# Optimization experiments

Hardware: AMD Instinct MI355X
Metric: run time of the kernel (lower is better)

The kernel has to match this reference:

```python
import jax, jax.numpy as jnp
import numpy as np

N = 200      # num_of_node
P = 200      # num_of_pattern
TOPK = 3
STRIDE = 25
B = 32
T = 9000     # S * STRIDE with S = 360
H = 128      # classifier hidden


def setup_inputs() -> dict:
    key = jax.random.key(0)
    k0, k1, k2, k3 = jax.random.split(key, 4)
    x = jax.random.normal(k0, (B, N, T), dtype=jnp.float32)
    # xavier_uniform-ish scale, gain 1.414
    patterns = jax.random.normal(k1, (P, N), dtype=jnp.float32) * np.float32(1.414 * np.sqrt(2.0 / (P + N)))
    W1 = jax.random.normal(k2, (N, H), dtype=jnp.float32) * np.float32(np.sqrt(2.0 / N))
    b1 = jnp.zeros((H,), jnp.float32)
    W2 = jax.random.normal(k3, (H, 2), dtype=jnp.float32) * np.float32(np.sqrt(2.0 / H))
    b2 = jnp.zeros((2,), jnp.float32)
    return {"x": x, "length": 9000, "patterns": patterns,
            "W1": W1, "b1": b1, "W2": W2, "b2": b2}


def _forward(x, patterns, W1, b1, W2, b2, length):
    Bx = x.shape[0]
    S = length // STRIDE                     # size_after_pool (static int)
    eye = jnp.eye(N, dtype=x.dtype)
    # patterns = tanh(patterns * (1 - I)) + I, then L2-normalize rows
    p = jnp.tanh(patterns * (1.0 - eye)) + eye
    np_ = p / jnp.sqrt((p ** 2).sum(-1, keepdims=True) + 1e-9)          # [P,N]
    # MRI_length_regularize: crop and transpose -> [B,T,N]
    frames = jnp.swapaxes(x[:, :, :S * STRIDE], 1, 2)
    nf = frames / jnp.sqrt((frames ** 2).sum(-1, keepdims=True) + 1e-9)  # [B,T,N]
    # cosine similarity frame vs pattern
    scores = jnp.einsum('btn,pn->btp', nf, np_)                          # [B,T,P]
    # MaxPool1d(stride, stride, return_indices=True) on [B,P,T]
    sw = jnp.swapaxes(scores, 1, 2).reshape(Bx, P, S, STRIDE)
    posscores = sw.max(-1)                                               # [B,P,S]
    negscores = (-sw).max(-1)
    offs = jnp.arange(S) * STRIDE
    pos_idx = jax.lax.stop_gradient(jnp.argmax(sw, -1) + offs)           # [B,P,S] global indices
    neg_idx = jax.lax.stop_gradient(jnp.argmax(-sw, -1) + offs)
    # scatter +1/-1 into signal_select [B,P,T]; indices unique per (b,p) row
    bidx = jnp.arange(Bx)[:, None, None]
    pidx = jnp.arange(P)[None, :, None]
    ss = jnp.zeros((Bx, P, S * STRIDE), x.dtype)
    ss = ss.at[bidx, pidx, pos_idx].add(1.0)
    ss = ss.at[bidx, pidx, neg_idx].add(-1.0)
    Sf = jnp.asarray(S, x.dtype)
    avg_sel = np.float32(np.sqrt(200.0 / TOPK)) * jnp.einsum('bpt,btn->bpn', ss, nf) / Sf / 2.0
    compos = (posscores / Sf).sum(-1)                                    # [B,P]
    comneg = (negscores / Sf).sum(-1)
    finalscore = (compos + comneg) / 2.0
    # top_select on normalized patterns (abs topK mask per row)
    idx = jax.lax.top_k(jnp.abs(np_), TOPK)[1]                           # [P,K]
    mask = jnp.zeros((P, N), x.dtype).at[jnp.arange(P)[:, None], idx].set(1.0)
    tp = mask * np_                                                      # toppattern [P,N]
    Tframe = avg_sel * mask                                              # [B,P,N]
    scores2 = ((Tframe / jnp.sqrt((Tframe ** 2).sum(-1, keepdims=True) + 1e-9)) *
               (tp / jnp.sqrt((tp ** 2).sum(-1, keepdims=True) + 1e-9))).sum(-1)  # [B,P]
    # SigLoss: Frobenius norms
    norm = (1.0 - jnp.sqrt((tp ** 2).sum()) / jnp.sqrt((np_ ** 2).sum())) ** 2
    # realpattern: sign(toppattern)/topK, detached
    rp = jax.lax.stop_gradient(jnp.sign(tp) / TOPK)                      # [P,N]
    non_diag = jnp.ones((N, N), x.dtype) * TOPK - eye * (TOPK - 1)
    diag = finalscore + 0.25 * (scores2 * np.float32(np.sqrt(TOPK / 200.0)))
    graphs = jnp.einsum('pn,bp,pm->bnm', rp, diag, rp) * non_diag / (TOPK / 5.0)  # [B,N,N]
    # Graph_Analysis('ae') stand-in classifier: per-node MLP + mean pool + linear head
    h = jax.nn.relu(graphs @ W1 + b1)                                    # [B,N,H]
    out = h.mean(1) @ W2 + b2                                            # [B,2]
    return out, norm, graphs


def reference(x, length, patterns, W1, b1, W2, b2):
    return _forward(x, patterns, W1, b1, W2, b2, length)
```

## Files before the change

kernel.cpp:

```cpp
#include <hip/hip_runtime.h>
#include <math.h>

namespace {

constexpr int kN = 200;
constexpr int kP = 200;
constexpr int kT = 9000;
constexpr int kB = 32;
constexpr int kS = 360;
constexpr int kH = 128;
constexpr int kWC = 72;


__device__ inline float wave_sum(float v) {
#pragma unroll
  for (int off = 32; off >= 1; off >>= 1) v += __shfl_xor(v, off);
  return v;
}

__global__ __launch_bounds__(64) void k_pattern(
    const float* __restrict__ pat, float* __restrict__ npm,
    float* __restrict__ t3val, int* __restrict__ t3idx,
    float* __restrict__ t3sign, float* __restrict__ ssq_tp,
    float* __restrict__ gsums) {
  const int p = blockIdx.x, lane = threadIdx.x;
  __shared__ float row[kN];
  float v[4];
  float ssq = 0.f;
#pragma unroll
  for (int j = 0; j < 4; ++j) {
    int n = lane + 64 * j;
    float val = 0.f;
    if (n < kN) {
      float a = pat[p * kN + n];
      val = (n == p) ? 1.0f : tanhf(a);
    }
    v[j] = val;
    ssq += val * val;
  }
  ssq = wave_sum(ssq);
  const float inv = 1.0f / sqrtf(ssq + 1e-9f);
  float ssqn = 0.f;
#pragma unroll
  for (int j = 0; j < 4; ++j) {
    int n = lane + 64 * j;
    if (n < kN) {
      float nv = v[j] * inv;
      npm[p * kN + n] = nv;
      row[n] = nv;
      ssqn += nv * nv;
    }
  }
  ssqn = wave_sum(ssqn);
  __syncthreads();
  if (lane == 0) {
    float v1 = -1.f, v2 = -1.f, v3 = -1.f;
    int i1 = 0, i2 = 0, i3 = 0;
    for (int n = 0; n < kN; ++n) {
      float a = fabsf(row[n]);
      if (a > v1)      { v3 = v2; i3 = i2; v2 = v1; i2 = i1; v1 = a; i1 = n; }
      else if (a > v2) { v3 = v2; i3 = i2; v2 = a; i2 = n; }
      else if (a > v3) { v3 = a; i3 = n; }
    }
    float a1 = row[i1], a2 = row[i2], a3 = row[i3];
    t3idx[p * 3 + 0] = i1; t3idx[p * 3 + 1] = i2; t3idx[p * 3 + 2] = i3;
    t3val[p * 3 + 0] = a1; t3val[p * 3 + 1] = a2; t3val[p * 3 + 2] = a3;
    t3sign[p * 3 + 0] = (a1 > 0.f) ? 1.f : ((a1 < 0.f) ? -1.f : 0.f);
    t3sign[p * 3 + 1] = (a2 > 0.f) ? 1.f : ((a2 < 0.f) ? -1.f : 0.f);
    t3sign[p * 3 + 2] = (a3 > 0.f) ? 1.f : ((a3 < 0.f) ? -1.f : 0.f);
    float st = a1 * a1 + a2 * a2 + a3 * a3;
    ssq_tp[p] = st;
    atomicAdd(&gsums[0], ssqn);
    atomicAdd(&gsums[1], st);
  }
}

__global__ __launch_bounds__(256) void k_rownorm(const float* __restrict__ x,
                                                 float* __restrict__ inv_rn) {
  int idx = blockIdx.x * 256 + threadIdx.x;
  if (idx >= kB * kT) return;
  int b = idx / kT, t = idx % kT;
  const float* xp = x + (size_t)b * kN * kT + t;
  float s0 = 0.f, s1 = 0.f, s2 = 0.f, s3 = 0.f;
  for (int n = 0; n < kN; n += 4) {
    float x0 = xp[(size_t)(n + 0) * kT];
    float x1 = xp[(size_t)(n + 1) * kT];
    float x2 = xp[(size_t)(n + 2) * kT];
    float x3 = xp[(size_t)(n + 3) * kT];
    s0 += x0 * x0; s1 += x1 * x1; s2 += x2 * x2; s3 += x3 * x3;
  }
  float s = (s0 + s1) + (s2 + s3);
  inv_rn[idx] = 1.0f / sqrtf(s + 1e-9f);
}

__global__ __launch_bounds__(512, 2) void k_scores_pool(
    const float* __restrict__ x, const float* __restrict__ npm,
    const float* __restrict__ inv_rn,
    float* __restrict__ posval, float* __restrict__ negval,
    unsigned short* __restrict__ posi, unsigned short* __restrict__ negi) {
  const int bid = blockIdx.x;
  const int b = bid / kWC, wc = bid % kWC;
  const int t0 = wc * 125;
  __shared__ float ps[kP * 51];
  __shared__ float xs[50 * 140];
  const int tid = threadIdx.x;
  const int p2 = tid % 100, w = tid / 100;
  const bool active = tid < 500;
  float accA[25], accB[25];
#pragma unroll
  for (int t = 0; t < 25; ++t) { accA[t] = 0.f; accB[t] = 0.f; }
  const size_t xb = (size_t)b * kN * kT;

  for (int nc = 0; nc < 4; ++nc) {
    __syncthreads();
    for (int i = tid; i < kP * 50; i += 512) {
      int p = i / 50, n = i % 50;
      ps[p * 51 + n] = npm[p * kN + nc * 50 + n];
    }
    for (int i = tid; i < 50 * 125; i += 512) {
      int n = i / 125, tt = i % 125;
      xs[n * 140 + (tt / 25) * 28 + (tt % 25)] =
          x[xb + (size_t)(nc * 50 + n) * kT + t0 + tt];
    }
    __syncthreads();
    if (active) {
      for (int n = 0; n < 50; ++n) {
        float va = ps[p2 * 51 + n];
        float vb = ps[(p2 + 100) * 51 + n];
        const float* xr = &xs[n * 140 + w * 28];
#pragma unroll
        for (int t = 0; t < 25; ++t) {
          float xv = xr[t];
          accA[t] = fmaf(va, xv, accA[t]);
          accB[t] = fmaf(vb, xv, accB[t]);
        }
      }
    }
  }

  if (active) {
    const int tg0 = t0 + w * 25;
    float bA = -1e30f, bnA = -1e30f, bB = -1e30f, bnB = -1e30f;
    int iA = 0, inA = 0, iB = 0, inB = 0;
#pragma unroll
    for (int t = 0; t < 25; ++t) {
      float iv = inv_rn[b * kT + tg0 + t];
      float sA = accA[t] * iv, sB = accB[t] * iv;
      if (sA > bA)   { bA = sA;  iA = t; }
      if (-sA > bnA) { bnA = -sA; inA = t; }
      if (sB > bB)   { bB = sB;  iB = t; }
      if (-sB > bnB) { bnB = -sB; inB = t; }
    }
    const int s = wc * 5 + w;
    const size_t oA = (size_t)(b * kP + p2) * kS + s;
    const size_t oB = (size_t)(b * kP + p2 + 100) * kS + s;
    posval[oA] = bA;  negval[oA] = bnA;
    posval[oB] = bB;  negval[oB] = bnB;
    posi[oA] = (unsigned short)(tg0 + iA);
    negi[oA] = (unsigned short)(tg0 + inA);
    posi[oB] = (unsigned short)(tg0 + iB);
    negi[oB] = (unsigned short)(tg0 + inB);
  }
}

__global__ __launch_bounds__(256) void k_avgsel(
    const float* __restrict__ x, const float* __restrict__ inv_rn,
    const unsigned short* __restrict__ posi, const unsigned short* __restrict__ negi,
    const float* __restrict__ posval, const float* __restrict__ negval,
    const int* __restrict__ t3idx, const float* __restrict__ t3val,
    const float* __restrict__ ssq_tp, float* __restrict__ diag) {
  const int gw = blockIdx.x * 4 + (threadIdx.x >> 6);
  const int lane = threadIdx.x & 63;
  const int b = gw / kP, p = gw % kP;
  const int n0 = t3idx[p * 3 + 0], n1 = t3idx[p * 3 + 1], n2 = t3idx[p * 3 + 2];
  const float* xb = x + (size_t)b * kN * kT;
  const float* ivb = inv_rn + b * kT;
  const size_t base = (size_t)(b * kP + p) * kS;
  float a0 = 0.f, a1 = 0.f, a2 = 0.f, sp = 0.f, sn = 0.f;
  for (int s = lane; s < kS; s += 64) {
    int tp_ = posi[base + s], tn_ = negi[base + s];
    float ivp = ivb[tp_], ivn = ivb[tn_];
    a0 += xb[(size_t)n0 * kT + tp_] * ivp - xb[(size_t)n0 * kT + tn_] * ivn;
    a1 += xb[(size_t)n1 * kT + tp_] * ivp - xb[(size_t)n1 * kT + tn_] * ivn;
    a2 += xb[(size_t)n2 * kT + tp_] * ivp - xb[(size_t)n2 * kT + tn_] * ivn;
    sp += posval[base + s];
    sn += negval[base + s];
  }
  a0 = wave_sum(a0); a1 = wave_sum(a1); a2 = wave_sum(a2);
  sp = wave_sum(sp); sn = wave_sum(sn);
  if (lane == 0) {
    const float c0 = 8.16496580927726f;
    float T0 = c0 * a0 / 360.0f / 2.0f;
    float T1 = c0 * a1 / 360.0f / 2.0f;
    float T2 = c0 * a2 / 360.0f / 2.0f;
    float st = T0 * T0 + T1 * T1 + T2 * T2;
    float itf = 1.0f / sqrtf(st + 1e-9f);
    float itp = 1.0f / sqrtf(ssq_tp[p] + 1e-9f);
    float s2 = T0 * itf * (t3val[p * 3 + 0] * itp) +
               T1 * itf * (t3val[p * 3 + 1] * itp) +
               T2 * itf * (t3val[p * 3 + 2] * itp);
    float fs = (sp / 360.0f + sn / 360.0f) * 0.5f;
    diag[b * kP + p] = fs + 0.25f * (s2 * 0.12247448713915890f);
  }
}

__global__ __launch_bounds__(256) void k_graphs(
    const float* __restrict__ diag, const int* __restrict__ t3idx,
    const float* __restrict__ t3sign, float* __restrict__ gout) {
  const int b = blockIdx.x, tid = threadIdx.x;
  __shared__ float g[kN * kN];
  for (int i = tid; i < kN * kN; i += 256) g[i] = 0.f;
  __syncthreads();
  for (int p = tid; p < kP; p += 256) {
    float d = diag[b * kP + p];
    int i0 = t3idx[p * 3 + 0], i1 = t3idx[p * 3 + 1], i2 = t3idx[p * 3 + 2];
    float r0 = t3sign[p * 3 + 0] * (1.0f / 3.0f);
    float r1 = t3sign[p * 3 + 1] * (1.0f / 3.0f);
    float r2 = t3sign[p * 3 + 2] * (1.0f / 3.0f);
    int   ii[3] = {i0, i1, i2};
    float rr[3] = {r0, r1, r2};
#pragma unroll
    for (int j = 0; j < 3; ++j)
#pragma unroll
      for (int k = 0; k < 3; ++k)
        atomicAdd(&g[ii[j] * kN + ii[k]], d * rr[j] * rr[k]);
  }
  __syncthreads();
  float* go = gout + (size_t)b * kN * kN;
  for (int i = tid; i < kN * kN; i += 256) {
    int n = i / kN, m = i % kN;
    float nd = (n == m) ? 1.0f : 3.0f;
    go[i] = g[i] * nd / 0.6f;
  }
}

__global__ __launch_bounds__(256) void k_classifier(
    const float* __restrict__ graphs, const float* __restrict__ W1,
    const float* __restrict__ b1, float* __restrict__ meanh) {
  const int b = blockIdx.x / 8, nc = blockIdx.x % 8;
  const int tid = threadIdx.x;
  __shared__ float g[25][kN];
  for (int i = tid; i < 25 * kN; i += 256) {
    int n = i / kN, m = i % kN;
    g[n][m] = graphs[(size_t)b * kN * kN + (size_t)(nc * 25 + n) * kN + m];
  }
  __syncthreads();
  const int hh = tid & 127, grp = tid >> 7;
  const int ns = (grp == 0) ? 0 : 13, ne = (grp == 0) ? 13 : 25;
  float sumh = 0.f;
  for (int n = ns; n < ne; ++n) {
    float acc = b1[hh];
    for (int m = 0; m < kN; ++m) acc = fmaf(g[n][m], W1[m * kH + hh], acc);
    sumh += fmaxf(acc, 0.f);
  }
  atomicAdd(&meanh[b * kH + hh], sumh);
}

__global__ __launch_bounds__(64) void k_final(
    const float* __restrict__ meanh, const float* __restrict__ W2,
    const float* __restrict__ b2, const float* __restrict__ gsums,
    float* __restrict__ out) {
  const int tid = threadIdx.x;
  if (tid < 64) {
    int b = tid >> 1, k = tid & 1;
    float acc = 0.f;
    for (int h = 0; h < kH; ++h) {
      float mv = meanh[b * kH + h] / 200.0f;
      acc = fmaf(mv, W2[h * 2 + k], acc);
    }
    out[b * 2 + k] = acc + b2[k];
  }
  if (tid == 0) {
    float r = 1.0f - sqrtf(gsums[1]) / sqrtf(gsums[0]);
    out[64] = r * r;
  }
}

}

extern "C" void kernel_launch(void* const* d_in, const int* in_sizes, int n_in,
                              void* d_out, int out_size, void* d_ws, size_t ws_size,
                              hipStream_t stream) {
  const float* x   = (const float*)d_in[0];
  const float* pat = (const float*)d_in[2];
  const float* W1  = (const float*)d_in[3];
  const float* b1  = (const float*)d_in[4];
  const float* W2  = (const float*)d_in[5];
  const float* b2  = (const float*)d_in[6];
  float* out = (float*)d_out;

  char* ws = (char*)d_ws;
  float* meanh  = (float*)(ws + 0);
  float* gsums  = (float*)(ws + 16384);
  float* diag   = (float*)(ws + 16400);
  float* ssqtp  = (float*)(ws + 42000);
  float* t3val  = (float*)(ws + 42800);
  float* t3sign = (float*)(ws + 45200);
  int*   t3idx  = (int*)(ws + 47600);
  float* npm    = (float*)(ws + 50000);
  float* invrn  = (float*)(ws + 210000);
  float* posval = (float*)(ws + 1362000);
  float* negval = (float*)(ws + 10578000);
  unsigned short* posi = (unsigned short*)(ws + 19794000);
  unsigned short* negi = (unsigned short*)(ws + 24402000);

  hipMemsetAsync(d_ws, 0, 16392, stream);
  k_pattern<<<kP, 64, 0, stream>>>(pat, npm, t3val, t3idx, t3sign, ssqtp, gsums);
  k_rownorm<<<(kB * kT) / 256, 256, 0, stream>>>(x, invrn);
  k_scores_pool<<<kB * kWC, 512, 0, stream>>>(x, npm, invrn, posval, negval, posi, negi);
  k_avgsel<<<(kB * kP) / 4, 256, 0, stream>>>(x, invrn, posi, negi, posval, negval,
                                              t3idx, t3val, ssqtp, diag);
  k_graphs<<<kB, 256, 0, stream>>>(diag, t3idx, t3sign, out + 65);
  k_classifier<<<kB * 8, 256, 0, stream>>>(out + 65, W1, b1, meanh);
  k_final<<<1, 64, 0, stream>>>(meanh, W2, b2, gsums, out);
}
```

Measured before the change: 902.5 us.

## Retile score+pool GEMM to 125-register tiles and fuse pooled sums via atomics

Rewrites the score and max-pool kernel so each thread accumulates a 25-pattern by 5-time register tile. Operands are loaded from transposed, float4-friendly shared layouts, and the pattern matrix is now stored transposed. Pooled max and min values are reduced with shuffles and summed into per-(b,p) accumulators with atomics, which drops the large posval/negval buffers and the re-read of them in avgsel. The graph kernel becomes a direct global atomic scatter after a memset of the output, replacing the per-batch shared-memory build and full write. The 125-float accumulator raises register pressure and may lower occupancy. Float atomics also make the sum order nondeterministic.

```diff
diff --git a/kernel.cpp b/kernel.cpp
--- a/kernel.cpp
+++ b/kernel.cpp
@@ -9,7 +9,6 @@
 constexpr int kB = 32;
 constexpr int kS = 360;
 constexpr int kH = 128;
-constexpr int kWC = 72;
 
 
 __device__ inline float wave_sum(float v) {
@@ -19,7 +18,7 @@
 }
 
 __global__ __launch_bounds__(64) void k_pattern(
-    const float* __restrict__ pat, float* __restrict__ npm,
+    const float* __restrict__ pat, float* __restrict__ npmT,
     float* __restrict__ t3val, int* __restrict__ t3idx,
     float* __restrict__ t3sign, float* __restrict__ ssq_tp,
     float* __restrict__ gsums) {
@@ -46,7 +45,7 @@
     int n = lane + 64 * j;
     if (n < kN) {
       float nv = v[j] * inv;
-      npm[p * kN + n] = nv;
+      npmT[n * kP + p] = nv;
       row[n] = nv;
       ssqn += nv * nv;
     }
@@ -93,80 +92,130 @@
   inv_rn[idx] = 1.0f / sqrtf(s + 1e-9f);
 }
 
-__global__ __launch_bounds__(512, 2) void k_scores_pool(
-    const float* __restrict__ x, const float* __restrict__ npm,
+__global__ __launch_bounds__(256) void k_scores_pool2(
+    const float* __restrict__ x, const float* __restrict__ npmT,
     const float* __restrict__ inv_rn,
-    float* __restrict__ posval, float* __restrict__ negval,
-    unsigned short* __restrict__ posi, unsigned short* __restrict__ negi) {
+    unsigned short* __restrict__ posi, unsigned short* __restrict__ negi,
+    float* __restrict__ compos, float* __restrict__ comneg) {
   const int bid = blockIdx.x;
-  const int b = bid / kWC, wc = bid % kWC;
-  const int t0 = wc * 125;
-  __shared__ float ps[kP * 51];
-  __shared__ float xs[50 * 140];
+  const int pg = bid & 1;
+  const int tc = (bid >> 1) % 30;
+  const int b  = bid / 60;
+  const int t0 = tc * 300;
   const int tid = threadIdx.x;
-  const int p2 = tid % 100, w = tid / 100;
-  const bool active = tid < 500;
-  float accA[25], accB[25];
-#pragma unroll
-  for (int t = 0; t < 25; ++t) { accA[t] = 0.f; accB[t] = 0.f; }
-  const size_t xb = (size_t)b * kN * kT;
-
-  for (int nc = 0; nc < 4; ++nc) {
+  const int wid = tid >> 6, lane = tid & 63;
+
+  __shared__ float xs[20 * 64 * 8];
+  __shared__ float ps[20 * 4 * 28];
+  __shared__ float ivs[300];
+
+  for (int i = tid; i < 300; i += 256) ivs[i] = inv_rn[b * kT + t0 + i];
+
+  float acc[125];
+#pragma unroll
+  for (int i = 0; i < 125; ++i) acc[i] = 0.f;
+
+  const size_t xb = (size_t)b * kN * kT + t0;
+
+  for (int c = 0; c < 10; ++c) {
     __syncthreads();
-    for (int i = tid; i < kP * 50; i += 512) {
-      int p = i / 50, n = i % 50;
-      ps[p * 51 + n] = npm[p * kN + nc * 50 + n];
-    }
-    for (int i = tid; i < 50 * 125; i += 512) {
-      int n = i / 125, tt = i % 125;
-      xs[n * 140 + (tt / 25) * 28 + (tt % 25)] =
-          x[xb + (size_t)(nc * 50 + n) * kT + t0 + tt];
+    for (int i = tid; i < 20 * 300; i += 256) {
+      int n = i / 300, tt = i % 300;
+      xs[n * 512 + (tt / 5) * 8 + (tt % 5)] =
+          x[xb + (size_t)(c * 20 + n) * kT + tt];
+    }
+    for (int i = tid; i < 20 * 100; i += 256) {
+      int n = i / 100, pp = i % 100;
+      ps[n * 112 + (pp / 25) * 28 + (pp % 25)] =
+          npmT[(c * 20 + n) * kP + pg * 100 + pp];
     }
     __syncthreads();
-    if (active) {
-      for (int n = 0; n < 50; ++n) {
-        float va = ps[p2 * 51 + n];
-        float vb = ps[(p2 + 100) * 51 + n];
-        const float* xr = &xs[n * 140 + w * 28];
-#pragma unroll
-        for (int t = 0; t < 25; ++t) {
-          float xv = xr[t];
-          accA[t] = fmaf(va, xv, accA[t]);
-          accB[t] = fmaf(vb, xv, accB[t]);
+    for (int n = 0; n < 20; ++n) {
+      const float4 x4 = *(const float4*)&xs[n * 512 + lane * 8];
+      const float xv4 = xs[n * 512 + lane * 8 + 4];
+      const float* pr = &ps[n * 112 + wid * 28];
+#pragma unroll
+      for (int g = 0; g < 6; ++g) {
+        const float4 p4 = *(const float4*)&pr[g * 4];
+        {
+          const float pv = p4.x; const int o = (g * 4 + 0) * 5;
+          acc[o+0]=fmaf(pv,x4.x,acc[o+0]); acc[o+1]=fmaf(pv,x4.y,acc[o+1]);
+          acc[o+2]=fmaf(pv,x4.z,acc[o+2]); acc[o+3]=fmaf(pv,x4.w,acc[o+3]);
+          acc[o+4]=fmaf(pv,xv4,acc[o+4]);
         }
-      }
-    }
-  }
-
-  if (active) {
-    const int tg0 = t0 + w * 25;
-    float bA = -1e30f, bnA = -1e30f, bB = -1e30f, bnB = -1e30f;
-    int iA = 0, inA = 0, iB = 0, inB = 0;
-#pragma unroll
-    for (int t = 0; t < 25; ++t) {
-      float iv = inv_rn[b * kT + tg0 + t];
-      float sA = accA[t] * iv, sB = accB[t] * iv;
-      if (sA > bA)   { bA = sA;  iA = t; }
-      if (-sA > bnA) { bnA = -sA; inA = t; }
-      if (sB > bB)   { bB = sB;  iB = t; }
-      if (-sB > bnB) { bnB = -sB; inB = t; }
-    }
-    const int s = wc * 5 + w;
-    const size_t oA = (size_t)(b * kP + p2) * kS + s;
-    const size_t oB = (size_t)(b * kP + p2 + 100) * kS + s;
-    posval[oA] = bA;  negval[oA] = bnA;
-    posval[oB] = bB;  negval[oB] = bnB;
-    posi[oA] = (unsigned short)(tg0 + iA);
-    negi[oA] = (unsigned short)(tg0 + inA);
-    posi[oB] = (unsigned short)(tg0 + iB);
-    negi[oB] = (unsigned short)(tg0 + inB);
+        {
+          const float pv = p4.y; const int o = (g * 4 + 1) * 5;
+          acc[o+0]=fmaf(pv,x4.x,acc[o+0]); acc[o+1]=fmaf(pv,x4.y,acc[o+1]);
+          acc[o+2]=fmaf(pv,x4.z,acc[o+2]); acc[o+3]=fmaf(pv,x4.w,acc[o+3]);
+          acc[o+4]=fmaf(pv,xv4,acc[o+4]);
+        }
+        {
+          const float pv = p4.z; const int o = (g * 4 + 2) * 5;
+          acc[o+0]=fmaf(pv,x4.x,acc[o+0]); acc[o+1]=fmaf(pv,x4.y,acc[o+1]);
+          acc[o+2]=fmaf(pv,x4.z,acc[o+2]); acc[o+3]=fmaf(pv,x4.w,acc[o+3]);
+          acc[o+4]=fmaf(pv,xv4,acc[o+4]);
+        }
+        {
+          const float pv = p4.w; const int o = (g * 4 + 3) * 5;
+          acc[o+0]=fmaf(pv,x4.x,acc[o+0]); acc[o+1]=fmaf(pv,x4.y,acc[o+1]);
+          acc[o+2]=fmaf(pv,x4.z,acc[o+2]); acc[o+3]=fmaf(pv,x4.w,acc[o+3]);
+          acc[o+4]=fmaf(pv,xv4,acc[o+4]);
+        }
+      }
+      {
+        const float pv = pr[24]; const int o = 24 * 5;
+        acc[o+0]=fmaf(pv,x4.x,acc[o+0]); acc[o+1]=fmaf(pv,x4.y,acc[o+1]);
+        acc[o+2]=fmaf(pv,x4.z,acc[o+2]); acc[o+3]=fmaf(pv,x4.w,acc[o+3]);
+        acc[o+4]=fmaf(pv,xv4,acc[o+4]);
+      }
+    }
+  }
+
+  if (lane < 60) {
+    const int w = lane / 5;
+    const int k5 = lane % 5;
+    float iv[5];
+#pragma unroll
+    for (int j = 0; j < 5; ++j) iv[j] = ivs[lane * 5 + j];
+    const int sidx = tc * 12 + w;
+    const int pwbase = pg * 100 + wid * 25;
+#pragma unroll
+    for (int pp = 0; pp < 25; ++pp) {
+      float mv = -1e30f, nv = 1e30f;
+      int mi = 0, ni = 0;
+#pragma unroll
+      for (int j = 0; j < 5; ++j) {
+        float s = acc[pp * 5 + j] * iv[j];
+        if (s > mv) { mv = s; mi = lane * 5 + j; }
+        if (s < nv) { nv = s; ni = lane * 5 + j; }
+      }
+      float bmv = -1e30f, bnv = 1e30f;
+      int bmi = 0, bni = 0;
+#pragma unroll
+      for (int k = 0; k < 5; ++k) {
+        float v  = __shfl(mv, w * 5 + k);
+        int   vi = __shfl(mi, w * 5 + k);
+        float u  = __shfl(nv, w * 5 + k);
+        int   ui = __shfl(ni, w * 5 + k);
+        if (v > bmv) { bmv = v; bmi = vi; }
+        if (u < bnv) { bnv = u; bni = ui; }
+      }
+      if (k5 == 0) {
+        const int p = pwbase + pp;
+        const size_t o = (size_t)(b * kP + p) * kS + sidx;
+        posi[o] = (unsigned short)(t0 + bmi);
+        negi[o] = (unsigned short)(t0 + bni);
+        atomicAdd(&compos[b * kP + p], bmv);
+        atomicAdd(&comneg[b * kP + p], -bnv);
+      }
+    }
   }
 }
 
 __global__ __launch_bounds__(256) void k_avgsel(
     const float* __restrict__ x, const float* __restrict__ inv_rn,
     const unsigned short* __restrict__ posi, const unsigned short* __restrict__ negi,
-    const float* __restrict__ posval, const float* __restrict__ negval,
+    const float* __restrict__ compos, const float* __restrict__ comneg,
     const int* __restrict__ t3idx, const float* __restrict__ t3val,
     const float* __restrict__ ssq_tp, float* __restrict__ diag) {
   const int gw = blockIdx.x * 4 + (threadIdx.x >> 6);
@@ -176,18 +225,15 @@
   const float* xb = x + (size_t)b * kN * kT;
   const float* ivb = inv_rn + b * kT;
   const size_t base = (size_t)(b * kP + p) * kS;
-  float a0 = 0.f, a1 = 0.f, a2 = 0.f, sp = 0.f, sn = 0.f;
+  float a0 = 0.f, a1 = 0.f, a2 = 0.f;
   for (int s = lane; s < kS; s += 64) {
     int tp_ = posi[base + s], tn_ = negi[base + s];
     float ivp = ivb[tp_], ivn = ivb[tn_];
     a0 += xb[(size_t)n0 * kT + tp_] * ivp - xb[(size_t)n0 * kT + tn_] * ivn;
     a1 += xb[(size_t)n1 * kT + tp_] * ivp - xb[(size_t)n1 * kT + tn_] * ivn;
     a2 += xb[(size_t)n2 * kT + tp_] * ivp - xb[(size_t)n2 * kT + tn_] * ivn;
-    sp += posval[base + s];
-    sn += negval[base + s];
   }
   a0 = wave_sum(a0); a1 = wave_sum(a1); a2 = wave_sum(a2);
-  sp = wave_sum(sp); sn = wave_sum(sn);
   if (lane == 0) {
     const float c0 = 8.16496580927726f;
     float T0 = c0 * a0 / 360.0f / 2.0f;
@@ -199,39 +245,33 @@
     float s2 = T0 * itf * (t3val[p * 3 + 0] * itp) +
                T1 * itf * (t3val[p * 3 + 1] * itp) +
                T2 * itf * (t3val[p * 3 + 2] * itp);
-    float fs = (sp / 360.0f + sn / 360.0f) * 0.5f;
+    float fs = (compos[b * kP + p] / 360.0f + comneg[b * kP + p] / 360.0f) * 0.5f;
     diag[b * kP + p] = fs + 0.25f * (s2 * 0.12247448713915890f);
   }
 }
 
-__global__ __launch_bounds__(256) void k_graphs(
+__global__ __launch_bounds__(256) void k_graphs_scatter(
     const float* __restrict__ diag, const int* __restrict__ t3idx,
     const float* __restrict__ t3sign, float* __restrict__ gout) {
-  const int b = blockIdx.x, tid = threadIdx.x;
-  __shared__ float g[kN * kN];
-  for (int i = tid; i < kN * kN; i += 256) g[i] = 0.f;
-  __syncthreads();
-  for (int p = tid; p < kP; p += 256) {
-    float d = diag[b * kP + p];
-    int i0 = t3idx[p * 3 + 0], i1 = t3idx[p * 3 + 1], i2 = t3idx[p * 3 + 2];
-    float r0 = t3sign[p * 3 + 0] * (1.0f / 3.0f);
-    float r1 = t3sign[p * 3 + 1] * (1.0f / 3.0f);
-    float r2 = t3sign[p * 3 + 2] * (1.0f / 3.0f);
-    int   ii[3] = {i0, i1, i2};
-    float rr[3] = {r0, r1, r2};
-#pragma unroll
-    for (int j = 0; j < 3; ++j)
-#pragma unroll
-      for (int k = 0; k < 3; ++k)
-        atomicAdd(&g[ii[j] * kN + ii[k]], d * rr[j] * rr[k]);
-  }
-  __syncthreads();
+  const int i = blockIdx.x * 256 + threadIdx.x;
+  if (i >= kB * kP) return;
+  const int b = i / kP, p = i % kP;
+  const float d = diag[i];
+  int   ii[3];
+  float rr[3];
+#pragma unroll
+  for (int j = 0; j < 3; ++j) {
+    ii[j] = t3idx[p * 3 + j];
+    rr[j] = t3sign[p * 3 + j] * (1.0f / 3.0f);
+  }
   float* go = gout + (size_t)b * kN * kN;
-  for (int i = tid; i < kN * kN; i += 256) {
-    int n = i / kN, m = i % kN;
-    float nd = (n == m) ? 1.0f : 3.0f;
-    go[i] = g[i] * nd / 0.6f;
-  }
+#pragma unroll
+  for (int j = 0; j < 3; ++j)
+#pragma unroll
+    for (int k = 0; k < 3; ++k) {
+      float nd = (ii[j] == ii[k]) ? 1.0f : 3.0f;
+      atomicAdd(&go[ii[j] * kN + ii[k]], d * rr[j] * rr[k] * nd * (1.0f / 0.6f));
+    }
 }
 
 __global__ __launch_bounds__(256) void k_classifier(
@@ -292,25 +332,29 @@
   char* ws = (char*)d_ws;
   float* meanh  = (float*)(ws + 0);
   float* gsums  = (float*)(ws + 16384);
-  float* diag   = (float*)(ws + 16400);
-  float* ssqtp  = (float*)(ws + 42000);
-  float* t3val  = (float*)(ws + 42800);
-  float* t3sign = (float*)(ws + 45200);
-  int*   t3idx  = (int*)(ws + 47600);
-  float* npm    = (float*)(ws + 50000);
-  float* invrn  = (float*)(ws + 210000);
-  float* posval = (float*)(ws + 1362000);
-  float* negval = (float*)(ws + 10578000);
-  unsigned short* posi = (unsigned short*)(ws + 19794000);
-  unsigned short* negi = (unsigned short*)(ws + 24402000);
-
-  hipMemsetAsync(d_ws, 0, 16392, stream);
-  k_pattern<<<kP, 64, 0, stream>>>(pat, npm, t3val, t3idx, t3sign, ssqtp, gsums);
-  k_rownorm<<<(kB * kT) / 256, 256, 0, stream>>>(x, invrn);
-  k_scores_pool<<<kB * kWC, 512, 0, stream>>>(x, npm, invrn, posval, negval, posi, negi);
-  k_avgsel<<<(kB * kP) / 4, 256, 0, stream>>>(x, invrn, posi, negi, posval, negval,
+  float* compos = (float*)(ws + 16400);
+  float* comneg = (float*)(ws + 42000);
+  float* diag   = (float*)(ws + 67600);
+  float* ssqtp  = (float*)(ws + 93200);
+  float* t3val  = (float*)(ws + 94000);
+  float* t3sign = (float*)(ws + 96400);
+  int*   t3idx  = (int*)(ws + 98800);
+  float* npmT   = (float*)(ws + 101200);
+  float* invrn  = (float*)(ws + 261200);
+  unsigned short* posi = (unsigned short*)(ws + 1413200);
+  unsigned short* negi = (unsigned short*)(ws + 6021200);
+
+  hipMemsetAsync(d_ws, 0, 67600, stream);
+  hipMemsetAsync((char*)d_out + 65 * 4, 0, (size_t)kB * kN * kN * 4, stream);
+
+  k_pattern<<<kP, 64, 0, stream>>>(pat, npmT, t3val, t3idx, t3sign, ssqtp, gsums);
+  k_rownorm<<<(kB * kT + 255) / 256, 256, 0, stream>>>(x, invrn);
+  k_scores_pool2<<<kB * 30 * 2, 256, 0, stream>>>(x, npmT, invrn, posi, negi,
+                                                  compos, comneg);
+  k_avgsel<<<(kB * kP) / 4, 256, 0, stream>>>(x, invrn, posi, negi, compos, comneg,
                                               t3idx, t3val, ssqtp, diag);
-  k_graphs<<<kB, 256, 0, stream>>>(diag, t3idx, t3sign, out + 65);
+  k_graphs_scatter<<<(kB * kP + 255) / 256, 256, 0, stream>>>(diag, t3idx, t3sign,
+                                                              out + 65);
   k_classifier<<<kB * 8, 256, 0, stream>>>(out + 65, W1, b1, meanh);
   k_final<<<1, 64, 0, stream>>>(meanh, W2, b2, gsums, out);
 }
```

Result: slower. 1.676 ms (+85.6%).

## Fuse row-norm, score pooling and selection averaging into one scores kernel

Applied to the files above, without the earlier changes.

Removes the separate row-norm pass over x by accumulating squared sums in shared memory while x tiles are staged. The pooled argmax/argmin results are consumed in place: each block gathers the top-3 node values and accumulates pooled sums into shared buffers, then flushes them with global atomics. This drops the large posval/negval/posi/negi intermediates and the avgsel kernel. The graph build becomes a per-(b,p) global atomic scatter onto a memset output. The costs are added shared-memory atomics during tile loading, the loss of the two-blocks-per-CU launch bound, and float-atomic ordering nondeterminism.

```diff
diff --git a/kernel.cpp b/kernel.cpp
--- a/kernel.cpp
+++ b/kernel.cpp
@@ -9,7 +9,6 @@
 constexpr int kB = 32;
 constexpr int kS = 360;
 constexpr int kH = 128;
-constexpr int kWC = 72;
 
 
 __device__ inline float wave_sum(float v) {
@@ -75,41 +74,34 @@
   }
 }
 
-__global__ __launch_bounds__(256) void k_rownorm(const float* __restrict__ x,
-                                                 float* __restrict__ inv_rn) {
-  int idx = blockIdx.x * 256 + threadIdx.x;
-  if (idx >= kB * kT) return;
-  int b = idx / kT, t = idx % kT;
-  const float* xp = x + (size_t)b * kN * kT + t;
-  float s0 = 0.f, s1 = 0.f, s2 = 0.f, s3 = 0.f;
-  for (int n = 0; n < kN; n += 4) {
-    float x0 = xp[(size_t)(n + 0) * kT];
-    float x1 = xp[(size_t)(n + 1) * kT];
-    float x2 = xp[(size_t)(n + 2) * kT];
-    float x3 = xp[(size_t)(n + 3) * kT];
-    s0 += x0 * x0; s1 += x1 * x1; s2 += x2 * x2; s3 += x3 * x3;
-  }
-  float s = (s0 + s1) + (s2 + s3);
-  inv_rn[idx] = 1.0f / sqrtf(s + 1e-9f);
-}
-
-__global__ __launch_bounds__(512, 2) void k_scores_pool(
+__global__ __launch_bounds__(512) void k_scores_fused(
     const float* __restrict__ x, const float* __restrict__ npm,
-    const float* __restrict__ inv_rn,
-    float* __restrict__ posval, float* __restrict__ negval,
-    unsigned short* __restrict__ posi, unsigned short* __restrict__ negi) {
+    const int* __restrict__ t3idx,
+    float* __restrict__ asumG, float* __restrict__ cposG,
+    float* __restrict__ cnegG) {
   const int bid = blockIdx.x;
-  const int b = bid / kWC, wc = bid % kWC;
+  const int b = bid / 72, wc = bid % 72;
   const int t0 = wc * 125;
   __shared__ float ps[kP * 51];
   __shared__ float xs[50 * 140];
+  __shared__ float ssq[128];
+  __shared__ float asumL[kP * 3];
+  __shared__ float cposL[kP];
+  __shared__ float cnegL[kP];
+  __shared__ int   t3iL[kP * 3];
   const int tid = threadIdx.x;
   const int p2 = tid % 100, w = tid / 100;
   const bool active = tid < 500;
+
+  for (int i = tid; i < kP * 3; i += 512) { asumL[i] = 0.f; t3iL[i] = t3idx[i]; }
+  for (int i = tid; i < kP; i += 512) { cposL[i] = 0.f; cnegL[i] = 0.f; }
+  for (int i = tid; i < 128; i += 512) ssq[i] = 0.f;
+
   float accA[25], accB[25];
 #pragma unroll
   for (int t = 0; t < 25; ++t) { accA[t] = 0.f; accB[t] = 0.f; }
-  const size_t xb = (size_t)b * kN * kT;
+  const size_t xbase = (size_t)b * kN * kT;
+  const size_t xb = xbase + t0;
 
   for (int nc = 0; nc < 4; ++nc) {
     __syncthreads();
@@ -119,8 +111,9 @@
     }
     for (int i = tid; i < 50 * 125; i += 512) {
       int n = i / 125, tt = i % 125;
-      xs[n * 140 + (tt / 25) * 28 + (tt % 25)] =
-          x[xb + (size_t)(nc * 50 + n) * kT + t0 + tt];
+      float v = x[xb + (size_t)(nc * 50 + n) * kT + tt];
+      xs[n * 140 + (tt / 25) * 28 + (tt % 25)] = v;
+      atomicAdd(&ssq[tt], v * v);
     }
     __syncthreads();
     if (active) {
@@ -140,98 +133,90 @@
 
   if (active) {
     const int tg0 = t0 + w * 25;
-    float bA = -1e30f, bnA = -1e30f, bB = -1e30f, bnB = -1e30f;
-    int iA = 0, inA = 0, iB = 0, inB = 0;
-#pragma unroll
-    for (int t = 0; t < 25; ++t) {
-      float iv = inv_rn[b * kT + tg0 + t];
-      float sA = accA[t] * iv, sB = accB[t] * iv;
-      if (sA > bA)   { bA = sA;  iA = t; }
-      if (-sA > bnA) { bnA = -sA; inA = t; }
-      if (sB > bB)   { bB = sB;  iB = t; }
-      if (-sB > bnB) { bnB = -sB; inB = t; }
-    }
-    const int s = wc * 5 + w;
-    const size_t oA = (size_t)(b * kP + p2) * kS + s;
-    const size_t oB = (size_t)(b * kP + p2 + 100) * kS + s;
-    posval[oA] = bA;  negval[oA] = bnA;
-    posval[oB] = bB;  negval[oB] = bnB;
-    posi[oA] = (unsigned short)(tg0 + iA);
-    negi[oA] = (unsigned short)(tg0 + inA);
-    posi[oB] = (unsigned short)(tg0 + iB);
-    negi[oB] = (unsigned short)(tg0 + inB);
-  }
-}
-
-__global__ __launch_bounds__(256) void k_avgsel(
-    const float* __restrict__ x, const float* __restrict__ inv_rn,
-    const unsigned short* __restrict__ posi, const unsigned short* __restrict__ negi,
-    const float* __restrict__ posval, const float* __restrict__ negval,
-    const int* __restrict__ t3idx, const float* __restrict__ t3val,
+    float iv[25];
+#pragma unroll
+    for (int t = 0; t < 25; ++t) iv[t] = 1.0f / sqrtf(ssq[w * 25 + t] + 1e-9f);
+
+#define DO_HALF(ACC, PIDX)                                                    \
+    {                                                                         \
+      const int P_ = (PIDX);                                                  \
+      float bmv = -1e30f, bnv = 1e30f, ivp = 0.f, ivn = 0.f;                  \
+      int bmi = 0, bni = 0;                                                   \
+      _Pragma("unroll")                                                       \
+      for (int t = 0; t < 25; ++t) {                                          \
+        float s = ACC[t] * iv[t];                                             \
+        if (s > bmv) { bmv = s; bmi = t; ivp = iv[t]; }                       \
+        if (s < bnv) { bnv = s; bni = t; ivn = iv[t]; }                       \
+      }                                                                       \
+      atomicAdd(&cposL[P_], bmv);                                             \
+      atomicAdd(&cnegL[P_], -bnv);                     \
+      const int gp = tg0 + bmi, gn = tg0 + bni;                               \
+      _Pragma("unroll")                                                       \
+      for (int j = 0; j < 3; ++j) {                                           \
+        int nj = t3iL[P_ * 3 + j];                                            \
+        float xpv = x[xbase + (size_t)nj * kT + gp];                          \
+        float xnv = x[xbase + (size_t)nj * kT + gn];                          \
+        atomicAdd(&asumL[P_ * 3 + j], xpv * ivp - xnv * ivn);                 \
+      }                                                                       \
+    }
+
+    DO_HALF(accA, p2)
+    DO_HALF(accB, p2 + 100)
+#undef DO_HALF
+  }
+
+  __syncthreads();
+  for (int i = tid; i < kP * 5; i += 512) {
+    if (i < kP * 3)           atomicAdd(&asumG[b * kP * 3 + i], asumL[i]);
+    else if (i < kP * 4)      atomicAdd(&cposG[b * kP + (i - kP * 3)], cposL[i - kP * 3]);
+    else                      atomicAdd(&cnegG[b * kP + (i - kP * 4)], cnegL[i - kP * 4]);
+  }
+}
+
+__global__ __launch_bounds__(256) void k_diag(
+    const float* __restrict__ asumG, const float* __restrict__ cposG,
+    const float* __restrict__ cnegG, const float* __restrict__ t3val,
     const float* __restrict__ ssq_tp, float* __restrict__ diag) {
-  const int gw = blockIdx.x * 4 + (threadIdx.x >> 6);
-  const int lane = threadIdx.x & 63;
-  const int b = gw / kP, p = gw % kP;
-  const int n0 = t3idx[p * 3 + 0], n1 = t3idx[p * 3 + 1], n2 = t3idx[p * 3 + 2];
-  const float* xb = x + (size_t)b * kN * kT;
-  const float* ivb = inv_rn + b * kT;
-  const size_t base = (size_t)(b * kP + p) * kS;
-  float a0 = 0.f, a1 = 0.f, a2 = 0.f, sp = 0.f, sn = 0.f;
-  for (int s = lane; s < kS; s += 64) {
-    int tp_ = posi[base + s], tn_ = negi[base + s];
-    float ivp = ivb[tp_], ivn = ivb[tn_];
-    a0 += xb[(size_t)n0 * kT + tp_] * ivp - xb[(size_t)n0 * kT + tn_] * ivn;
-    a1 += xb[(size_t)n1 * kT + tp_] * ivp - xb[(size_t)n1 * kT + tn_] * ivn;
-    a2 += xb[(size_t)n2 * kT + tp_] * ivp - xb[(size_t)n2 * kT + tn_] * ivn;
-    sp += posval[base + s];
-    sn += negval[base + s];
-  }
-  a0 = wave_sum(a0); a1 = wave_sum(a1); a2 = wave_sum(a2);
-  sp = wave_sum(sp); sn = wave_sum(sn);
-  if (lane == 0) {
-    const float c0 = 8.16496580927726f;
-    float T0 = c0 * a0 / 360.0f / 2.0f;
-    float T1 = c0 * a1 / 360.0f / 2.0f;
-    float T2 = c0 * a2 / 360.0f / 2.0f;
-    float st = T0 * T0 + T1 * T1 + T2 * T2;
-    float itf = 1.0f / sqrtf(st + 1e-9f);
-    float itp = 1.0f / sqrtf(ssq_tp[p] + 1e-9f);
-    float s2 = T0 * itf * (t3val[p * 3 + 0] * itp) +
-               T1 * itf * (t3val[p * 3 + 1] * itp) +
-               T2 * itf * (t3val[p * 3 + 2] * itp);
-    float fs = (sp / 360.0f + sn / 360.0f) * 0.5f;
-    diag[b * kP + p] = fs + 0.25f * (s2 * 0.12247448713915890f);
-  }
-}
-
-__global__ __launch_bounds__(256) void k_graphs(
+  const int i = blockIdx.x * 256 + threadIdx.x;
+  if (i >= kB * kP) return;
+  const int p = i % kP;
+  const float c0 = 8.16496580927726f;
+  float a0 = asumG[i * 3 + 0], a1 = asumG[i * 3 + 1], a2 = asumG[i * 3 + 2];
+  float T0 = c0 * a0 / 360.0f / 2.0f;
+  float T1 = c0 * a1 / 360.0f / 2.0f;
+  float T2 = c0 * a2 / 360.0f / 2.0f;
+  float st = T0 * T0 + T1 * T1 + T2 * T2;
+  float itf = 1.0f / sqrtf(st + 1e-9f);
+  float itp = 1.0f / sqrtf(ssq_tp[p] + 1e-9f);
+  float s2 = T0 * itf * (t3val[p * 3 + 0] * itp) +
+             T1 * itf * (t3val[p * 3 + 1] * itp) +
+             T2 * itf * (t3val[p * 3 + 2] * itp);
+  float fs = (cposG[i] / 360.0f + cnegG[i] / 360.0f) * 0.5f;
+  diag[i] = fs + 0.25f * (s2 * 0.12247448713915890f);
+}
+
+__global__ __launch_bounds__(256) void k_graphs_scatter(
     const float* __restrict__ diag, const int* __restrict__ t3idx,
     const float* __restrict__ t3sign, float* __restrict__ gout) {
-  const int b = blockIdx.x, tid = threadIdx.x;
-  __shared__ float g[kN * kN];
-  for (int i = tid; i < kN * kN; i += 256) g[i] = 0.f;
-  __syncthreads();
-  for (int p = tid; p < kP; p += 256) {
-    float d = diag[b * kP + p];
-    int i0 = t3idx[p * 3 + 0], i1 = t3idx[p * 3 + 1], i2 = t3idx[p * 3 + 2];
-    float r0 = t3sign[p * 3 + 0] * (1.0f / 3.0f);
-    float r1 = t3sign[p * 3 + 1] * (1.0f / 3.0f);
-    float r2 = t3sign[p * 3 + 2] * (1.0f / 3.0f);
-    int   ii[3] = {i0, i1, i2};
-    float rr[3] = {r0, r1, r2};
-#pragma unroll
-    for (int j = 0; j < 3; ++j)
-#pragma unroll
-      for (int k = 0; k < 3; ++k)
-        atomicAdd(&g[ii[j] * kN + ii[k]], d * rr[j] * rr[k]);
-  }
-  __syncthreads();
+  const int i = blockIdx.x * 256 + threadIdx.x;
+  if (i >= kB * kP) return;
+  const int b = i / kP, p = i % kP;
+  const float d = diag[i];
+  int   ii[3];
+  float rr[3];
+#pragma unroll
+  for (int j = 0; j < 3; ++j) {
+    ii[j] = t3idx[p * 3 + j];
+    rr[j] = t3sign[p * 3 + j] * (1.0f / 3.0f);
+  }
   float* go = gout + (size_t)b * kN * kN;
-  for (int i = tid; i < kN * kN; i += 256) {
-    int n = i / kN, m = i % kN;
-    float nd = (n == m) ? 1.0f : 3.0f;
-    go[i] = g[i] * nd / 0.6f;
-  }
+#pragma unroll
+  for (int j = 0; j < 3; ++j)
+#pragma unroll
+    for (int k = 0; k < 3; ++k) {
+      float nd = (ii[j] == ii[k]) ? 1.0f : 3.0f;
+      atomicAdd(&go[ii[j] * kN + ii[k]], d * rr[j] * rr[k] * nd * (1.0f / 0.6f));
+    }
 }
 
 __global__ __launch_bounds__(256) void k_classifier(
@@ -290,27 +275,27 @@
   float* out = (float*)d_out;
 
   char* ws = (char*)d_ws;
-  float* meanh  = (float*)(ws + 0);
-  float* gsums  = (float*)(ws + 16384);
-  float* diag   = (float*)(ws + 16400);
-  float* ssqtp  = (float*)(ws + 42000);
-  float* t3val  = (float*)(ws + 42800);
-  float* t3sign = (float*)(ws + 45200);
-  int*   t3idx  = (int*)(ws + 47600);
-  float* npm    = (float*)(ws + 50000);
-  float* invrn  = (float*)(ws + 210000);
-  float* posval = (float*)(ws + 1362000);
-  float* negval = (float*)(ws + 10578000);
-  unsigned short* posi = (unsigned short*)(ws + 19794000);
-  unsigned short* negi = (unsigned short*)(ws + 24402000);
-
-  hipMemsetAsync(d_ws, 0, 16392, stream);
+  float* gsums  = (float*)(ws + 0);
+  float* meanh  = (float*)(ws + 64);
+  float* cpos   = (float*)(ws + 16448);
+  float* cneg   = (float*)(ws + 42048);
+  float* asum   = (float*)(ws + 67648);
+  float* diag   = (float*)(ws + 144448);
+  float* ssqtp  = (float*)(ws + 170048);
+  float* t3val  = (float*)(ws + 170848);
+  float* t3sign = (float*)(ws + 173248);
+  int*   t3idx  = (int*)(ws + 175648);
+  float* npm    = (float*)(ws + 178048);
+
+  hipMemsetAsync(d_ws, 0, 144448, stream);
+  hipMemsetAsync((char*)d_out + 65 * 4, 0, (size_t)kB * kN * kN * 4, stream);
+
   k_pattern<<<kP, 64, 0, stream>>>(pat, npm, t3val, t3idx, t3sign, ssqtp, gsums);
-  k_rownorm<<<(kB * kT) / 256, 256, 0, stream>>>(x, invrn);
-  k_scores_pool<<<kB * kWC, 512, 0, stream>>>(x, npm, invrn, posval, negval, posi, negi);
-  k_avgsel<<<(kB * kP) / 4, 256, 0, stream>>>(x, invrn, posi, negi, posval, negval,
-                                              t3idx, t3val, ssqtp, diag);
-  k_graphs<<<kB, 256, 0, stream>>>(diag, t3idx, t3sign, out + 65);
+  k_scores_fused<<<kB * 72, 512, 0, stream>>>(x, npm, t3idx, asum, cpos, cneg);
+  k_diag<<<(kB * kP + 255) / 256, 256, 0, stream>>>(asum, cpos, cneg, t3val,
+                                                    ssqtp, diag);
+  k_graphs_scatter<<<(kB * kP + 255) / 256, 256, 0, stream>>>(diag, t3idx, t3sign,
+                                                              out + 65);
   k_classifier<<<kB * 8, 256, 0, stream>>>(out + 65, W1, b1, meanh);
   k_final<<<1, 64, 0, stream>>>(meanh, W2, b2, gsums, out);
 }
```

Measured after the change: 954.2 us. 1.06x slower.
